# Kernel optimization log

Measured on AMD Instinct MI355X. Metric: run time of the kernel, lower is better.

The kernel has to match this reference:

```python
import jax, jax.numpy as jnp
import numpy as np

N, E = 10000, 320000
C = 64          # channel multiplicity of 0e and 1o node features
A = 4           # node_attrs (species one-hot) dim
NB = 8          # radial basis size (edge_embedding dim)
H = 8           # invariant_neurons
AVG_NEIGH = 32.0
LOG2 = 0.6931471805599453

def ssp(x):
    # ShiftedSoftPlus
    return jax.nn.softplus(x) - LOG2


def setup_inputs() -> dict:
    key = jax.random.key(0)
    ks = jax.random.split(key, 13)
    d = dict(
        node_features=jax.random.normal(ks[0], (N, 4 * C), jnp.float32),   # [N, C + 3C]
        node_attrs=jax.random.normal(ks[1], (N, A), jnp.float32),
        edge_attrs=jax.random.normal(ks[2], (E, 4), jnp.float32),          # sh l=0,1
        edge_embedding=jax.random.uniform(ks[3], (E, NB), jnp.float32),
        edge_index=jax.random.randint(ks[4], (2, E), 0, N),
        # e3nn Linear (internal weights) per-l blocks
        W_lin1_0=jax.random.normal(ks[5], (C, C), jnp.float32),
        W_lin1_1=jax.random.normal(ks[6], (C, C), jnp.float32),
        # radial FullyConnectedNet: NB -> H -> 4C (tp.weight_numel)
        W_fc1=jax.random.normal(ks[7], (NB, H), jnp.float32),
        W_fc2=jax.random.normal(ks[8], (H, 4 * C), jnp.float32),
        # linear_2: irreps_mid.simplify() = 2Cx0e+2Cx1o -> Cx0e+Cx1o
        W_lin2_0=jax.random.normal(ks[9], (2 * C, C), jnp.float32),
        W_lin2_1=jax.random.normal(ks[10], (2 * C, C), jnp.float32),
        # self-connection FullyConnectedTensorProduct weights (node_attrs are scalars)
        W_sc0=jax.random.normal(ks[11], (C, A, C), jnp.float32),
        W_sc1=jax.random.normal(ks[12], (C, A, C), jnp.float32),
    )
    return d


def _forward(node_features, node_attrs, edge_attrs, edge_embedding, edge_index,
             W_lin1_0, W_lin1_1, W_fc1, W_fc2, W_lin2_0, W_lin2_1, W_sc0, W_sc1):
    n = node_features.shape[0]
    e = edge_attrs.shape[0]
    x0 = node_features[:, :C]                      # [N, C]   scalars (0e)
    x1 = node_features[:, C:].reshape(n, C, 3)     # [N, C, 3] vectors (1o)

    # self-connection: FullyConnectedTensorProduct(feat, node_attrs(0e)) -> feat
    sc_norm = 1.0 / np.sqrt(C * A)
    sc0 = jnp.einsum('nu,na,uav->nv', x0, node_attrs, W_sc0) * sc_norm
    sc1 = jnp.einsum('num,na,uav->nvm', x1, node_attrs, W_sc1) * sc_norm

    # linear_1 (per-irrep mixing, e3nn normalization 1/sqrt(fan_in))
    y0 = (x0 @ W_lin1_0) / np.sqrt(C)
    y1 = jnp.einsum('num,uv->nvm', x1, W_lin1_1) / np.sqrt(C)

    # radial MLP -> per-edge TP weights [E, 4C] (instruction order p1..p4)
    h = ssp((edge_embedding @ W_fc1) / np.sqrt(NB))
    w = (h @ W_fc2) / np.sqrt(H)
    wp1, wp2, wp3, wp4 = jnp.split(w, 4, axis=1)   # each [E, C]

    src = edge_index[1]
    dst = edge_index[0]
    xs0 = y0[src]                                  # [E, C]
    xs1 = y1[src]                                  # [E, C, 3]
    sh0 = edge_attrs[:, :1]                        # [E, 1]
    sh1 = edge_attrs[:, 1:4]                       # [E, 3]

    # uvu tensor product paths (component normalization)
    mid_s0 = wp1 * xs0 * sh0                                            # 0e x 0e -> 0e
    mid_s1 = wp4 * jnp.einsum('eum,em->eu', xs1, sh1) / np.sqrt(3.0)    # 1o x 1o -> 0e
    mid_v0 = (wp2 * xs0)[:, :, None] * sh1[:, None, :]                  # 0e x 1o -> 1o
    mid_v1 = wp3[:, :, None] * xs1 * sh0[:, :, None]                    # 1o x 0e -> 1o

    edge_feat = jnp.concatenate(
        [mid_s0, mid_s1, mid_v0.reshape(e, 3 * C), mid_v1.reshape(e, 3 * C)], axis=1
    )                                                                    # [E, 8C]

    # scatter-sum to destination nodes, then divide by sqrt(avg_num_neighbors)
    agg = jnp.zeros((n, 8 * C), edge_feat.dtype).at[dst].add(edge_feat)
    agg = agg / np.sqrt(AVG_NEIGH)

    s = agg[:, :2 * C]                              # [N, 2C] scalars
    v = agg[:, 2 * C:].reshape(n, 2 * C, 3)         # [N, 2C, 3] vectors

    # linear_2 on simplified mid irreps
    o0 = (s @ W_lin2_0) / np.sqrt(2 * C) + sc0
    o1 = jnp.einsum('num,uv->nvm', v, W_lin2_1) / np.sqrt(2 * C) + sc1

    return jnp.concatenate([o0, o1.reshape(n, 3 * C)], axis=1)          # [N, 4C]


def reference(node_features, node_attrs, edge_attrs, edge_embedding, edge_index,
              W_lin1_0, W_lin1_1, W_fc1, W_fc2, W_lin2_0, W_lin2_1, W_sc0, W_sc1):
    return _forward(node_features, node_attrs, edge_attrs, edge_embedding, edge_index,
                    W_lin1_0, W_lin1_1, W_fc1, W_fc2, W_lin2_0, W_lin2_1, W_sc0, W_sc1)
```

## Files before the change

kernel.cpp:

```cpp
#include <hip/hip_runtime.h>


__device__ __forceinline__ unsigned short f2b(float f) {
  unsigned u = __float_as_uint(f);
  return (unsigned short)((u + 0x7FFFu + ((u >> 16) & 1u)) >> 16);
}
__device__ __forceinline__ unsigned packb(float a, float b) {
  return (unsigned)f2b(a) | ((unsigned)f2b(b) << 16);
}
__device__ __forceinline__ float blo(unsigned p) { return __uint_as_float(p << 16); }
__device__ __forceinline__ float bhi(unsigned p) { return __uint_as_float(p & 0xFFFF0000u); }
__device__ __forceinline__ float b2f(unsigned short h) {
  return __uint_as_float((unsigned)h << 16);
}

__global__ __launch_bounds__(256) void k_pack(
    const float* __restrict__ W10, const float* __restrict__ W11,
    const float* __restrict__ Ws0, const float* __restrict__ Ws1,
    const float* __restrict__ W20, const float* __restrict__ W21,
    unsigned* __restrict__ wpk1, unsigned* __restrict__ wpks,
    unsigned* __restrict__ wpk2a, unsigned* __restrict__ wpk2b) {
  int i = blockIdx.x * 256 + threadIdx.x;
  if (i < 4096) wpk1[i] = packb(W10[i], W11[i]);
  else if (i < 4096 + 16384) {
    int j = i - 4096;
    wpks[j] = packb(Ws0[j], Ws1[j]);
  } else if (i < 4096 + 16384 + 4096) {
    int j = i - (4096 + 16384);
    wpk2a[j] = packb(W20[j], W20[4096 + j]);
  } else if (i < 4096 + 16384 + 8192) {
    int j = i - (4096 + 16384 + 4096);
    wpk2b[j] = packb(W21[j], W21[4096 + j]);
  }
}

__global__ __launch_bounds__(256) void k_hist(const int* __restrict__ ei,
                                              int* __restrict__ cnt, int nedges) {
  int e = blockIdx.x * 256 + threadIdx.x;
  if (e < nedges) atomicAdd(&cnt[ei[e]], 1);
}

__global__ __launch_bounds__(1024) void k_scan(const int* __restrict__ cnt,
                                               int* __restrict__ offs,
                                               int* __restrict__ cur,
                                               int nnodes, int nedges) {
  __shared__ int s_wtot[16], s_wpre[16];
  const int tid = threadIdx.x;
  const int lane = tid & 63;
  const int w = tid >> 6;
  int vals[16];
  int tot = 0;
  const int start = tid * 16;
#pragma unroll
  for (int k = 0; k < 16; ++k) {
    int i = start + k;
    int c = (i < nnodes) ? cnt[i] : 0;
    vals[k] = c;
    tot += c;
  }
  int incl = tot;
#pragma unroll
  for (int off = 1; off < 64; off <<= 1) {
    int v = __shfl_up(incl, off, 64);
    if (lane >= off) incl += v;
  }
  if (lane == 63) s_wtot[w] = incl;
  __syncthreads();
  if (tid == 0) {
    int run = 0;
#pragma unroll
    for (int i = 0; i < 16; ++i) { s_wpre[i] = run; run += s_wtot[i]; }
  }
  __syncthreads();
  int run = s_wpre[w] + (incl - tot);
#pragma unroll
  for (int k = 0; k < 16; ++k) {
    int i = start + k;
    if (i < nnodes) {
      offs[i] = run;
      cur[i] = run;
      run += vals[k];
    }
  }
  if (tid == 0) offs[nnodes] = nedges;
}

__global__ __launch_bounds__(256) void k_build(
    const int* __restrict__ ei, const float* __restrict__ ee,
    const float* __restrict__ ea, const float* __restrict__ Wf1,
    int* __restrict__ cur, int* __restrict__ srcs,
    uint4* __restrict__ erec, int nedges) {
  __shared__ float s_w[64];
  const int tid = threadIdx.x;
  if (tid < 64) s_w[tid] = Wf1[tid];
  __syncthreads();
  int e = blockIdx.x * 256 + tid;
  if (e >= nedges) return;
  const int d = ei[e];
  const int s = ei[nedges + e];
  const int p = atomicAdd(&cur[d], 1);
  srcs[p] = s;
  const float4 a = *(const float4*)(ee + (size_t)e * 8);
  const float4 b = *(const float4*)(ee + (size_t)e * 8 + 4);
  float r[8];
  const float is8 = 0.35355339059327379f;
#pragma unroll
  for (int j = 0; j < 8; ++j) {
    float dd = a.x * s_w[0 * 8 + j] + a.y * s_w[1 * 8 + j] + a.z * s_w[2 * 8 + j] +
               a.w * s_w[3 * 8 + j] + b.x * s_w[4 * 8 + j] + b.y * s_w[5 * 8 + j] +
               b.z * s_w[6 * 8 + j] + b.w * s_w[7 * 8 + j];
    dd *= is8;
    float sp = fmaxf(dd, 0.f) + log1pf(__expf(-fabsf(dd)));
    r[j] = (sp - 0.69314718055994531f) * is8;
  }
  const float4 sh = *(const float4*)(ea + (size_t)e * 4);
  erec[(size_t)p * 2] = make_uint4(packb(r[0], r[1]), packb(r[2], r[3]),
                                   packb(r[4], r[5]), packb(r[6], r[7]));
  erec[(size_t)p * 2 + 1] =
      make_uint4(__float_as_uint(sh.x), __float_as_uint(sh.y),
                 __float_as_uint(sh.z), __float_as_uint(sh.w));
}

__global__ __launch_bounds__(1024) void k_node_pre(
    const float* __restrict__ nf, const float* __restrict__ na,
    const unsigned* __restrict__ wpk1, const unsigned* __restrict__ wpks,
    unsigned short* __restrict__ yqb, float* __restrict__ out, int nnodes) {
  __shared__ unsigned s_w1[4096];
  __shared__ unsigned s_ws[16384];
  __shared__ unsigned short s_nfb[64][256];
  __shared__ float s_na[64][4];
  const int tid = threadIdx.x;
  const int lane = tid & 63;
  const int wv = tid >> 6;

  for (int i = tid; i < 4096; i += 1024) s_w1[i] = wpk1[i];
  for (int i = tid; i < 16384; i += 1024) s_ws[i] = wpks[i];

  const int ngroups = (nnodes + 63) / 64;
  for (int g = blockIdx.x; g < ngroups; g += gridDim.x) {
    const int base = g * 64;
    __syncthreads();
    for (int i = tid; i < 64 * 256; i += 1024) {
      int r = i >> 8, c = i & 255;
      int n = base + r;
      s_nfb[r][c] = (n < nnodes) ? f2b(nf[(size_t)n * 256 + c]) : (unsigned short)0;
    }
    if (tid < 256) {
      int r = tid >> 2, c = tid & 3;
      int n = base + r;
      s_na[r][c] = (n < nnodes) ? na[(size_t)n * 4 + c] : 0.f;
    }
    __syncthreads();

    const int r0 = wv * 4;
    const int v = lane;
    float y0a[4] = {0.f, 0.f, 0.f, 0.f};
    float y1a[4][3] = {};
    float sc0a[4] = {0.f, 0.f, 0.f, 0.f};
    float sc1a[4][3] = {};

#pragma unroll 2
    for (int u = 0; u < 64; ++u) {
      float x0r[4], x1r[4][3];
#pragma unroll
      for (int r = 0; r < 4; ++r) {
        x0r[r] = b2f(s_nfb[r0 + r][u]);
#pragma unroll
        for (int m = 0; m < 3; ++m) x1r[r][m] = b2f(s_nfb[r0 + r][64 + u * 3 + m]);
      }
      const unsigned q1 = s_w1[u * 64 + v];
      const float w0 = blo(q1);
      const float w1 = bhi(q1);
#pragma unroll
      for (int r = 0; r < 4; ++r) {
        y0a[r] = fmaf(x0r[r], w0, y0a[r]);
#pragma unroll
        for (int m = 0; m < 3; ++m) y1a[r][m] = fmaf(x1r[r][m], w1, y1a[r][m]);
      }
#pragma unroll
      for (int a = 0; a < 4; ++a) {
        const unsigned qs = s_ws[(u * 4 + a) * 64 + v];
        const float ws0 = blo(qs);
        const float ws1 = bhi(qs);
#pragma unroll
        for (int r = 0; r < 4; ++r) {
          const float nav = s_na[r0 + r][a];
          sc0a[r] = fmaf(x0r[r] * nav, ws0, sc0a[r]);
          const float t = nav * ws1;
#pragma unroll
          for (int m = 0; m < 3; ++m)
            sc1a[r][m] = fmaf(x1r[r][m], t, sc1a[r][m]);
        }
      }
    }

#pragma unroll
    for (int r = 0; r < 4; ++r) {
      const int n = base + r0 + r;
      if (n < nnodes) {
        ushort4 yv;
        yv.x = f2b(y0a[r] * 0.125f);
        yv.y = f2b(y1a[r][0] * 0.125f);
        yv.z = f2b(y1a[r][1] * 0.125f);
        yv.w = f2b(y1a[r][2] * 0.125f);
        *(ushort4*)(yqb + ((size_t)n * 64 + v) * 4) = yv;
        out[(size_t)n * 256 + v] = sc0a[r] * 0.0625f;
#pragma unroll
        for (int m = 0; m < 3; ++m)
          out[(size_t)n * 256 + 64 + v * 3 + m] = sc1a[r][m] * 0.0625f;
      }
    }
  }
}

__global__ __launch_bounds__(256, 4) void k_agg(
    const unsigned short* __restrict__ yqb, const uint4* __restrict__ erec,
    const int* __restrict__ srcs, const int* __restrict__ offs,
    const float* __restrict__ Wf2, unsigned short* __restrict__ aggb, int nnodes) {
  const int tid = threadIdx.x;
  const int u = tid & 63;
  const int wv = tid >> 6;
  const int n = blockIdx.x * 4 + wv;
  if (n >= nnodes) return;

  float wreg[32];
#pragma unroll
  for (int j = 0; j < 8; ++j)
#pragma unroll
    for (int q = 0; q < 4; ++q) wreg[j * 4 + q] = Wf2[j * 256 + q * 64 + u];

  float as0 = 0.f, as1 = 0.f;
  float av0[3] = {0.f, 0.f, 0.f};
  float av1[3] = {0.f, 0.f, 0.f};

  const int beg = offs[n], end = offs[n + 1];
#pragma unroll 4
  for (int i = beg; i < end; ++i) {
    const int src = srcs[i];
    const ushort4 yb = *(const ushort4*)(yqb + ((size_t)src * 64 + u) * 4);
    const uint4 hp = erec[(size_t)i * 2];
    const uint4 shu = erec[(size_t)i * 2 + 1];
    const float4 sh = make_float4(__uint_as_float(shu.x), __uint_as_float(shu.y),
                                  __uint_as_float(shu.z), __uint_as_float(shu.w));
    const float hv[8] = {blo(hp.x), bhi(hp.x), blo(hp.y), bhi(hp.y),
                         blo(hp.z), bhi(hp.z), blo(hp.w), bhi(hp.w)};
    float wp[4] = {0.f, 0.f, 0.f, 0.f};
#pragma unroll
    for (int j = 0; j < 8; ++j)
#pragma unroll
      for (int q = 0; q < 4; ++q) wp[q] = fmaf(hv[j], wreg[j * 4 + q], wp[q]);
    const float y0 = b2f(yb.x), y1 = b2f(yb.y), y2 = b2f(yb.z), y3 = b2f(yb.w);
    const float dot3 = y1 * sh.y + y2 * sh.z + y3 * sh.w;
    as0 = fmaf(wp[0] * y0, sh.x, as0);
    as1 = fmaf(wp[3], dot3, as1);
    const float t2 = wp[1] * y0;
    av0[0] = fmaf(t2, sh.y, av0[0]);
    av0[1] = fmaf(t2, sh.z, av0[1]);
    av0[2] = fmaf(t2, sh.w, av0[2]);
    const float t3 = wp[2] * sh.x;
    av1[0] = fmaf(t3, y1, av1[0]);
    av1[1] = fmaf(t3, y2, av1[1]);
    av1[2] = fmaf(t3, y3, av1[2]);
  }

  unsigned short* ap = aggb + (size_t)n * 512;
  ap[u] = f2b(as0);
  ap[64 + u] = f2b(as1 * 0.57735026918962576f);
#pragma unroll
  for (int m = 0; m < 3; ++m) {
    ap[128 + m * 64 + u] = f2b(av0[m]);
    ap[320 + m * 64 + u] = f2b(av1[m]);
  }
}

__global__ __launch_bounds__(256, 4) void k_lin2(
    const unsigned short* __restrict__ aggb, const unsigned* __restrict__ wpk2a,
    const unsigned* __restrict__ wpk2b, float* __restrict__ out, int nnodes) {
  __shared__ float s_x[4][4][512];
  const int tid = threadIdx.x;
  const int u = tid & 63;
  const int wv = tid >> 6;
  const int nb = blockIdx.x * 16 + wv * 4;

#pragma unroll
  for (int r = 0; r < 4; ++r) {
    const int n = nb + r;
    if (n < nnodes) {
      const uint4 aw = *(const uint4*)(aggb + (size_t)n * 512 + u * 8);
      float4* dst = (float4*)&s_x[wv][r][u * 8];
      dst[0] = make_float4(blo(aw.x), bhi(aw.x), blo(aw.y), bhi(aw.y));
      dst[1] = make_float4(blo(aw.z), bhi(aw.z), blo(aw.w), bhi(aw.w));
    }
  }

  float o0[4] = {0.f, 0.f, 0.f, 0.f};
  float o1[4][3] = {};

#pragma unroll 2
  for (int up = 0; up < 64; ++up) {
    const unsigned qa = wpk2a[up * 64 + u];
    const unsigned qb = wpk2b[up * 64 + u];
    const float w20a = blo(qa), w20b = bhi(qa);
    const float w21a = blo(qb), w21b = bhi(qb);
#pragma unroll
    for (int r = 0; r < 4; ++r) {
      o0[r] = fmaf(s_x[wv][r][up], w20a, o0[r]);
      o0[r] = fmaf(s_x[wv][r][64 + up], w20b, o0[r]);
#pragma unroll
      for (int m = 0; m < 3; ++m) {
        o1[r][m] = fmaf(s_x[wv][r][128 + m * 64 + up], w21a, o1[r][m]);
        o1[r][m] = fmaf(s_x[wv][r][320 + m * 64 + up], w21b, o1[r][m]);
      }
    }
  }

  const float scl = 1.f / 64.f;
#pragma unroll
  for (int r = 0; r < 4; ++r) {
    const int n = nb + r;
    if (n < nnodes) {
      out[(size_t)n * 256 + u] += o0[r] * scl;
#pragma unroll
      for (int m = 0; m < 3; ++m)
        out[(size_t)n * 256 + 64 + u * 3 + m] += o1[r][m] * scl;
    }
  }
}

extern "C" void kernel_launch(void* const* d_in, const int* in_sizes, int n_in,
                              void* d_out, int out_size, void* d_ws, size_t ws_size,
                              hipStream_t stream) {
  const float* nf = (const float*)d_in[0];
  const float* na = (const float*)d_in[1];
  const float* ea = (const float*)d_in[2];
  const float* ee = (const float*)d_in[3];
  const int* ei = (const int*)d_in[4];
  const float* W10 = (const float*)d_in[5];
  const float* W11 = (const float*)d_in[6];
  const float* Wf1 = (const float*)d_in[7];
  const float* Wf2 = (const float*)d_in[8];
  const float* W20 = (const float*)d_in[9];
  const float* W21 = (const float*)d_in[10];
  const float* Ws0 = (const float*)d_in[11];
  const float* Ws1 = (const float*)d_in[12];
  float* out = (float*)d_out;

  const int N = in_sizes[1] / 4;
  const int E = in_sizes[2] / 4;

  char* w = (char*)d_ws;
  auto carve = [&](size_t bytes) {
    char* p = w;
    w += (bytes + 255) & ~(size_t)255;
    return p;
  };
  unsigned short* yqb = (unsigned short*)carve((size_t)N * 256 * 2);
  uint4* erec = (uint4*)carve((size_t)E * 32);
  unsigned short* aggb = (unsigned short*)carve((size_t)N * 512 * 2);
  unsigned* wpk1 = (unsigned*)carve(4096 * 4);
  unsigned* wpks = (unsigned*)carve(16384 * 4);
  unsigned* wpk2a = (unsigned*)carve(4096 * 4);
  unsigned* wpk2b = (unsigned*)carve(4096 * 4);
  int* cnt = (int*)carve((size_t)N * sizeof(int));
  int* offs = (int*)carve((size_t)(N + 1) * sizeof(int));
  int* cur = (int*)carve((size_t)N * sizeof(int));
  int* srcs = (int*)carve((size_t)E * sizeof(int));

  hipMemsetAsync(cnt, 0, (size_t)N * sizeof(int), stream);
  k_pack<<<(4096 + 16384 + 8192 + 255) / 256, 256, 0, stream>>>(
      W10, W11, Ws0, Ws1, W20, W21, wpk1, wpks, wpk2a, wpk2b);
  const int egrid = (E + 255) / 256;
  k_hist<<<egrid, 256, 0, stream>>>(ei, cnt, E);
  k_scan<<<1, 1024, 0, stream>>>(cnt, offs, cur, N, E);
  k_build<<<egrid, 256, 0, stream>>>(ei, ee, ea, Wf1, cur, srcs, erec, E);
  const int ngroups = (N + 63) / 64;
  k_node_pre<<<ngroups, 1024, 0, stream>>>(nf, na, wpk1, wpks, yqb, out, N);
  k_agg<<<(N + 3) / 4, 256, 0, stream>>>(yqb, erec, srcs, offs, Wf2, aggb, N);
  k_lin2<<<(N + 15) / 16, 256, 0, stream>>>(aggb, wpk2a, wpk2b, out, N);
}
```

Measured before the change: 299.1 us.

## Repack node features and self-connection weights for vector LDS loads; stage lin2 weights

The self-connection weights are reordered so two species entries sit in one uint2, and node features are stored in LDS as ushort4 (scalar plus three vector components per channel). This lets k_node_pre fetch them with wider, fewer shared-memory reads, and node_attrs are hoisted into registers. k_lin2 now copies its packed weights into shared memory once per block instead of reading them from global memory in the inner loop. The trade-off is an extra 32KB of LDS in k_lin2, which may reduce occupancy, plus a strided global gather when filling the feature tile.

```diff
diff --git a/kernel.cpp b/kernel.cpp
--- a/kernel.cpp
+++ b/kernel.cpp
@@ -24,7 +24,8 @@
   if (i < 4096) wpk1[i] = packb(W10[i], W11[i]);
   else if (i < 4096 + 16384) {
     int j = i - 4096;
-    wpks[j] = packb(Ws0[j], Ws1[j]);
+    int u = j >> 8, a = (j >> 6) & 3, v = j & 63;
+    wpks[((u * 2 + (a >> 1)) * 64 + v) * 2 + (a & 1)] = packb(Ws0[j], Ws1[j]);
   } else if (i < 4096 + 16384 + 4096) {
     int j = i - (4096 + 16384);
     wpk2a[j] = packb(W20[j], W20[4096 + j]);
@@ -126,24 +127,35 @@
     const unsigned* __restrict__ wpk1, const unsigned* __restrict__ wpks,
     unsigned short* __restrict__ yqb, float* __restrict__ out, int nnodes) {
   __shared__ unsigned s_w1[4096];
-  __shared__ unsigned s_ws[16384];
-  __shared__ unsigned short s_nfb[64][256];
+  __shared__ uint2 s_ws2[8192];
+  __shared__ ushort4 s_nfb[64][64];
   __shared__ float s_na[64][4];
   const int tid = threadIdx.x;
   const int lane = tid & 63;
   const int wv = tid >> 6;
 
   for (int i = tid; i < 4096; i += 1024) s_w1[i] = wpk1[i];
-  for (int i = tid; i < 16384; i += 1024) s_ws[i] = wpks[i];
+  {
+    const uint2* wsrc = (const uint2*)wpks;
+    for (int i = tid; i < 8192; i += 1024) s_ws2[i] = wsrc[i];
+  }
 
   const int ngroups = (nnodes + 63) / 64;
   for (int g = blockIdx.x; g < ngroups; g += gridDim.x) {
     const int base = g * 64;
     __syncthreads();
-    for (int i = tid; i < 64 * 256; i += 1024) {
-      int r = i >> 8, c = i & 255;
+    for (int i = tid; i < 64 * 64; i += 1024) {
+      int r = i >> 6, u = i & 63;
       int n = base + r;
-      s_nfb[r][c] = (n < nnodes) ? f2b(nf[(size_t)n * 256 + c]) : (unsigned short)0;
+      ushort4 t = make_ushort4(0, 0, 0, 0);
+      if (n < nnodes) {
+        const float* row = nf + (size_t)n * 256;
+        t.x = f2b(row[u]);
+        t.y = f2b(row[64 + u * 3]);
+        t.z = f2b(row[64 + u * 3 + 1]);
+        t.w = f2b(row[64 + u * 3 + 2]);
+      }
+      s_nfb[r][u] = t;
     }
     if (tid < 256) {
       int r = tid >> 2, c = tid & 3;
@@ -154,6 +166,12 @@
 
     const int r0 = wv * 4;
     const int v = lane;
+    float nav[4][4];
+#pragma unroll
+    for (int r = 0; r < 4; ++r)
+#pragma unroll
+      for (int a = 0; a < 4; ++a) nav[r][a] = s_na[r0 + r][a];
+
     float y0a[4] = {0.f, 0.f, 0.f, 0.f};
     float y1a[4][3] = {};
     float sc0a[4] = {0.f, 0.f, 0.f, 0.f};
@@ -164,9 +182,11 @@
       float x0r[4], x1r[4][3];
 #pragma unroll
       for (int r = 0; r < 4; ++r) {
-        x0r[r] = b2f(s_nfb[r0 + r][u]);
-#pragma unroll
-        for (int m = 0; m < 3; ++m) x1r[r][m] = b2f(s_nfb[r0 + r][64 + u * 3 + m]);
+        const ushort4 xv = s_nfb[r0 + r][u];
+        x0r[r] = b2f(xv.x);
+        x1r[r][0] = b2f(xv.y);
+        x1r[r][1] = b2f(xv.z);
+        x1r[r][2] = b2f(xv.w);
       }
       const unsigned q1 = s_w1[u * 64 + v];
       const float w0 = blo(q1);
@@ -178,18 +198,22 @@
         for (int m = 0; m < 3; ++m) y1a[r][m] = fmaf(x1r[r][m], w1, y1a[r][m]);
       }
 #pragma unroll
-      for (int a = 0; a < 4; ++a) {
-        const unsigned qs = s_ws[(u * 4 + a) * 64 + v];
-        const float ws0 = blo(qs);
-        const float ws1 = bhi(qs);
-#pragma unroll
-        for (int r = 0; r < 4; ++r) {
-          const float nav = s_na[r0 + r][a];
-          sc0a[r] = fmaf(x0r[r] * nav, ws0, sc0a[r]);
-          const float t = nav * ws1;
-#pragma unroll
-          for (int m = 0; m < 3; ++m)
-            sc1a[r][m] = fmaf(x1r[r][m], t, sc1a[r][m]);
+      for (int a2 = 0; a2 < 2; ++a2) {
+        const uint2 q = s_ws2[(u * 2 + a2) * 64 + v];
+#pragma unroll
+        for (int half = 0; half < 2; ++half) {
+          const unsigned qq = half ? q.y : q.x;
+          const int a = a2 * 2 + half;
+          const float ws0 = blo(qq);
+          const float ws1 = bhi(qq);
+#pragma unroll
+          for (int r = 0; r < 4; ++r) {
+            sc0a[r] = fmaf(x0r[r] * nav[r][a], ws0, sc0a[r]);
+            const float t = nav[r][a] * ws1;
+#pragma unroll
+            for (int m = 0; m < 3; ++m)
+              sc1a[r][m] = fmaf(x1r[r][m], t, sc1a[r][m]);
+          }
         }
       }
     }
@@ -277,11 +301,16 @@
     const unsigned short* __restrict__ aggb, const unsigned* __restrict__ wpk2a,
     const unsigned* __restrict__ wpk2b, float* __restrict__ out, int nnodes) {
   __shared__ float s_x[4][4][512];
+  __shared__ unsigned s_w2[8192];
   const int tid = threadIdx.x;
   const int u = tid & 63;
   const int wv = tid >> 6;
   const int nb = blockIdx.x * 16 + wv * 4;
 
+  for (int i = tid; i < 4096; i += 256) {
+    s_w2[i] = wpk2a[i];
+    s_w2[4096 + i] = wpk2b[i];
+  }
 #pragma unroll
   for (int r = 0; r < 4; ++r) {
     const int n = nb + r;
@@ -292,14 +321,15 @@
       dst[1] = make_float4(blo(aw.z), bhi(aw.z), blo(aw.w), bhi(aw.w));
     }
   }
+  __syncthreads();
 
   float o0[4] = {0.f, 0.f, 0.f, 0.f};
   float o1[4][3] = {};
 
 #pragma unroll 2
   for (int up = 0; up < 64; ++up) {
-    const unsigned qa = wpk2a[up * 64 + u];
-    const unsigned qb = wpk2b[up * 64 + u];
+    const unsigned qa = s_w2[up * 64 + u];
+    const unsigned qb = s_w2[4096 + up * 64 + u];
     const float w20a = blo(qa), w20b = bhi(qa);
     const float w21a = blo(qb), w21b = bhi(qb);
 #pragma unroll
```

Measured after the change: 287.7 us. 3.8% less time.
